# Kernel tuning notes

Measured on AMD Instinct MI355X. Metric: run time of the kernel, lower is better.

## Reference

```python
import jax, jax.numpy as jnp
import numpy as np


def setup_inputs() -> dict:
    key = jax.random.key(0)
    k1, k2, k3, k4, k5 = jax.random.split(key, 5)
    B, C, D = 16384, 1000, 2048
    x = jax.random.normal(k1, (B, D), dtype=jnp.float32)
    W = jax.random.normal(k2, (C, D), dtype=jnp.float32) * 0.02  # fc weight
    b = jax.random.normal(k3, (C,), dtype=jnp.float32) * 0.01
    selector_weights = jax.random.normal(k4, (5,), dtype=jnp.float32) * 0.01
    selector_thresholds = jax.random.normal(k5, (5,), dtype=jnp.float32) * 0.01
    ensemble_threshold = jnp.zeros((1,), dtype=jnp.float32)
    return {
        "x": x, "W": W, "b": b,
        "selector_weights": selector_weights,
        "selector_thresholds": selector_thresholds,
        "ensemble_threshold": ensemble_threshold,
    }


def _selector_scores(logits, W):
    # top-2 of raw logits (RLConfM): sorted descending -> top_k(2)
    top2, _ = jax.lax.top_k(logits, 2)
    conf_m = top2[:, 0] - top2[:, 1]
    # geometric margin (RLGeoM): logits normalized by row norms of fc weight
    w_norms = jnp.linalg.norm(W, axis=1)                      # [C]
    norm_logits = logits / (w_norms + 1e-8)[None, :]          # [B, C]
    ntop2, _ = jax.lax.top_k(norm_logits, 2)
    geo_m = ntop2[:, 0] - ntop2[:, 1]
    # softmax-based selectors share one softmax pass
    probs = jax.nn.softmax(logits, axis=1)                    # [B, C]
    sr_max = jnp.max(probs, axis=1)
    doctor = 1.0 - 1.0 / jnp.sum(probs * probs, axis=1)
    neg_entropy = jnp.sum(probs * jnp.log(probs + 1e-10), axis=1)  # = -entropy
    # order matches nn.ModuleList: [SRMax, SRDoctor, SREntropy, RLGeoM, RLConfM]
    return jnp.stack([sr_max, doctor, neg_entropy, geo_m, conf_m], axis=1)  # [B, 5]


def reference(x, W, b, selector_weights, selector_thresholds, ensemble_threshold):
    # base model runs under no_grad in the original
    logits = jax.lax.stop_gradient(jnp.dot(x, W.T) + b)       # [B, C]
    scores = _selector_scores(logits, jax.lax.stop_gradient(W))  # [B, 5]
    indicators = jnp.tanh(scores - selector_thresholds[None, :])  # [B, 5]
    ensemble = jnp.sum(selector_weights[None, :] * indicators, axis=1)  # [B]
    selection_score = jnp.tanh(ensemble - ensemble_threshold[0])
    return (logits, selection_score)
```

## Files before the change

kernel.cpp:

```cpp
#include <hip/hip_runtime.h>
#include <stdint.h>

#define B_ROWS 16384
#define C_COLS 1000
#define D_DIM  2048

typedef __bf16 bf16x8 __attribute__((ext_vector_type(8)));
typedef float  f32x4  __attribute__((ext_vector_type(4)));
typedef unsigned short u16;

__device__ __forceinline__ u16 f2bf(float f) {
  union { float f; uint32_t u; } v; v.f = f;
  return (u16)((v.u + 0x7FFFu + ((v.u >> 16) & 1u)) >> 16);
}

__global__ __launch_bounds__(256)
void prep(const float* __restrict__ W, const float* __restrict__ x,
          u16* __restrict__ Wb, u16* __restrict__ xb, float* __restrict__ norms) {
  const int r = blockIdx.x;
  const int t = threadIdx.x;
  const bool isW = (r < C_COLS);
  const float* src = isW ? (W + (size_t)r * D_DIM)
                         : (x + (size_t)(r - C_COLS) * D_DIM);
  u16* dst = isW ? (Wb + (size_t)r * D_DIM)
                 : (xb + (size_t)(r - C_COLS) * D_DIM);
  const int c = t * 8;
  float4 v0 = *reinterpret_cast<const float4*>(src + c);
  float4 v1 = *reinterpret_cast<const float4*>(src + c + 4);
  uint32_t p0 = (uint32_t)f2bf(v0.x) | ((uint32_t)f2bf(v0.y) << 16);
  uint32_t p1 = (uint32_t)f2bf(v0.z) | ((uint32_t)f2bf(v0.w) << 16);
  uint32_t p2 = (uint32_t)f2bf(v1.x) | ((uint32_t)f2bf(v1.y) << 16);
  uint32_t p3 = (uint32_t)f2bf(v1.z) | ((uint32_t)f2bf(v1.w) << 16);
  const int row_id = isW ? r : (r - C_COLS);
  const int m2 = (row_id & 7) << 3;
  uint4 val; val.x = p0; val.y = p1; val.z = p2; val.w = p3;
  *reinterpret_cast<uint4*>(dst + (c ^ m2)) = val;
  if (isW) {
    float ss = v0.x*v0.x + v0.y*v0.y + v0.z*v0.z + v0.w*v0.w
             + v1.x*v1.x + v1.y*v1.y + v1.z*v1.z + v1.w*v1.w;
    #pragma unroll
    for (int m = 32; m; m >>= 1) ss += __shfl_xor(ss, m);
    __shared__ float wss[4];
    if ((t & 63) == 0) wss[t >> 6] = ss;
    __syncthreads();
    if (t == 0) norms[r] = sqrtf(wss[0] + wss[1] + wss[2] + wss[3]);
  }
}

#define ABASE(B,H) (((B)*2+(H))*8192)
#define BBASE(B,H) (32768 + ((B)*2+(H))*8192)

#define STAGE_A(BUF,H,KT) { _Pragma("unroll") for (int j_=0;j_<2;++j_){ \
    const char* s_ = (const char*)xb + \
      (((size_t)(m0+(H)*128+j_*64+w*8+(l>>3)))*D_DIM + (KT)*64 + (l&7)*8)*2; \
    u16* d_ = lds + ABASE(BUF,H) + (j_*64 + w*8)*64; \
    __builtin_amdgcn_global_load_lds( \
      (const __attribute__((address_space(1))) void*)s_, \
      (__attribute__((address_space(3))) void*)d_, 16, 0, 0); } }

#define STAGE_B(BUF,H,KT) { _Pragma("unroll") for (int j_=0;j_<2;++j_){ \
    int gr_ = n0+(H)*128+j_*64+w*8+(l>>3); if (gr_ >= C_COLS) gr_ = C_COLS-1; \
    const char* s_ = (const char*)Wb + \
      (((size_t)gr_)*D_DIM + (KT)*64 + (l&7)*8)*2; \
    u16* d_ = lds + BBASE(BUF,H) + (j_*64 + w*8)*64; \
    __builtin_amdgcn_global_load_lds( \
      (const __attribute__((address_space(1))) void*)s_, \
      (__attribute__((address_space(3))) void*)d_, 16, 0, 0); } }

#define READ_A(BUF,MH) { _Pragma("unroll") for (int ks_=0;ks_<2;++ks_) \
  _Pragma("unroll") for (int fr_=0;fr_<4;++fr_){ \
    int ra_ = wr*64 + fr_*16 + (l&15); \
    int ca_ = (ks_*32 + ((l>>4)<<3)) ^ ((ra_&7)<<3); \
    Acur[ks_][fr_] = *reinterpret_cast<const bf16x8*>( \
        &lds[ABASE(BUF,MH) + ra_*64 + ca_]); } }

#define READ_B(BUF,NH,DST) { _Pragma("unroll") for (int ks_=0;ks_<2;++ks_) \
  _Pragma("unroll") for (int fc_=0;fc_<2;++fc_){ \
    int rb_ = wcn*32 + fc_*16 + (l&15); \
    int cb_ = (ks_*32 + ((l>>4)<<3)) ^ ((rb_&7)<<3); \
    DST[ks_][fc_] = *reinterpret_cast<const bf16x8*>( \
        &lds[BBASE(BUF,NH) + rb_*64 + cb_]); } }

#define MMA(MH,NH,BSRC) { \
  __builtin_amdgcn_s_setprio(1); \
  _Pragma("unroll") for (int ks_=0;ks_<2;++ks_) \
    _Pragma("unroll") for (int fr_=0;fr_<4;++fr_) \
      _Pragma("unroll") for (int fc_=0;fc_<2;++fc_) \
        acc[MH][fr_][NH][fc_] = __builtin_amdgcn_mfma_f32_16x16x32_bf16( \
            Acur[ks_][fr_], BSRC[ks_][fc_], acc[MH][fr_][NH][fc_], 0, 0, 0); \
  __builtin_amdgcn_s_setprio(0); }

#define BAR  __builtin_amdgcn_s_barrier()
#define LG0  asm volatile("s_waitcnt lgkmcnt(0)" ::: "memory")
#define LG8  asm volatile("s_waitcnt lgkmcnt(8)" ::: "memory")
#define SCHB __builtin_amdgcn_sched_barrier(0)
#define VM4  asm volatile("s_waitcnt vmcnt(4)" ::: "memory")
#define VM0  asm volatile("s_waitcnt vmcnt(0)" ::: "memory")

__global__ __launch_bounds__(512, 2)
void gemm8(const u16* __restrict__ xb, const u16* __restrict__ Wb,
           const float* __restrict__ bias, float* __restrict__ out) {
  __shared__ u16 lds[65536];

  const int bid = blockIdx.x;
  const int swz = (bid & 7) * 32 + (bid >> 3);
  const int tm = swz >> 2, tn = swz & 3;
  const int m0 = tm * 256, n0 = tn * 256;

  const int t = threadIdx.x, w = t >> 6, l = t & 63;
  const int wr = w >> 2, wcn = w & 3;

  f32x4 acc[2][4][2][2];
  #pragma unroll
  for (int a = 0; a < 2; ++a)
    #pragma unroll
    for (int b2 = 0; b2 < 4; ++b2)
      #pragma unroll
      for (int c2 = 0; c2 < 2; ++c2)
        #pragma unroll
        for (int d2 = 0; d2 < 2; ++d2)
          acc[a][b2][c2][d2] = (f32x4){0.f, 0.f, 0.f, 0.f};

  bf16x8 Acur[2][4], B0c[2][2], B1c[2][2];

  STAGE_A(0,0,0); STAGE_B(0,0,0); STAGE_A(0,1,0); STAGE_B(0,1,0);
  STAGE_A(1,0,1); STAGE_B(1,0,1);
  VM4;
  BAR;

  for (int it = 0; it < 15; ++it) {
    const int t1k = 2*it + 1, t2k = 2*it + 2, t3k = 2*it + 3;
    READ_A(0,0); READ_B(0,0,B0c); STAGE_A(1,1,t1k); LG8;
    BAR; LG0; SCHB; MMA(0,0,B0c); BAR;
    READ_B(0,1,B1c); STAGE_B(1,1,t1k);
    BAR; LG0; SCHB; MMA(0,1,B1c); BAR;
    READ_A(0,1); STAGE_A(0,0,t2k);
    BAR; LG0; SCHB; MMA(1,1,B1c); BAR;
    STAGE_B(0,0,t2k);
    BAR; SCHB; MMA(1,0,B0c); VM4; BAR;
    READ_A(1,0); READ_B(1,0,B0c); STAGE_A(0,1,t2k); LG8;
    BAR; LG0; SCHB; MMA(0,0,B0c); BAR;
    READ_B(1,1,B1c); STAGE_B(0,1,t2k);
    BAR; LG0; SCHB; MMA(0,1,B1c); BAR;
    READ_A(1,1); STAGE_A(1,0,t3k);
    BAR; LG0; SCHB; MMA(1,1,B1c); BAR;
    STAGE_B(1,0,t3k);
    BAR; SCHB; MMA(1,0,B0c); VM4; BAR;
  }
  READ_A(0,0); READ_B(0,0,B0c); STAGE_A(1,1,31); LG8;
  BAR; LG0; SCHB; MMA(0,0,B0c); BAR;
  READ_B(0,1,B1c); STAGE_B(1,1,31);
  BAR; LG0; SCHB; MMA(0,1,B1c); BAR;
  READ_A(0,1);
  BAR; LG0; SCHB; MMA(1,1,B1c); BAR;
  BAR; SCHB; MMA(1,0,B0c); VM0; BAR;
  READ_A(1,0); READ_B(1,0,B0c); LG8;
  BAR; LG0; SCHB; MMA(0,0,B0c); BAR;
  READ_B(1,1,B1c);
  BAR; LG0; SCHB; MMA(0,1,B1c); BAR;
  READ_A(1,1);
  BAR; LG0; SCHB; MMA(1,1,B1c); BAR;
  SCHB; MMA(1,0,B0c);

  #pragma unroll
  for (int mh = 0; mh < 2; ++mh)
    #pragma unroll
    for (int nh = 0; nh < 2; ++nh)
      #pragma unroll
      for (int fc = 0; fc < 2; ++fc) {
        int col = n0 + nh*128 + wcn*32 + fc*16 + (l & 15);
        if (col < C_COLS) {
          float bv = bias[col];
          #pragma unroll
          for (int fr = 0; fr < 4; ++fr) {
            int row0 = m0 + mh*128 + wr*64 + fr*16 + ((l >> 4) << 2);
            #pragma unroll
            for (int j = 0; j < 4; ++j)
              out[(size_t)(row0 + j) * C_COLS + col] = acc[mh][fr][nh][fc][j] + bv;
          }
        }
      }
}

__global__ __launch_bounds__(256)
void prep_w_fb(const float* __restrict__ W, u16* __restrict__ Wb,
               float* __restrict__ norms) {
  const int r = blockIdx.x;
  const int t = threadIdx.x;
  const float* row = W + (size_t)r * D_DIM;
  const int c = t * 8;
  float4 v0 = *reinterpret_cast<const float4*>(row + c);
  float4 v1 = *reinterpret_cast<const float4*>(row + c + 4);
  float ss = v0.x*v0.x + v0.y*v0.y + v0.z*v0.z + v0.w*v0.w
           + v1.x*v1.x + v1.y*v1.y + v1.z*v1.z + v1.w*v1.w;
  uint32_t p0 = (uint32_t)f2bf(v0.x) | ((uint32_t)f2bf(v0.y) << 16);
  uint32_t p1 = (uint32_t)f2bf(v0.z) | ((uint32_t)f2bf(v0.w) << 16);
  uint32_t p2 = (uint32_t)f2bf(v1.x) | ((uint32_t)f2bf(v1.y) << 16);
  uint32_t p3 = (uint32_t)f2bf(v1.z) | ((uint32_t)f2bf(v1.w) << 16);
  const int mask = (r & 7) << 3;
  uint4 val; val.x = p0; val.y = p1; val.z = p2; val.w = p3;
  *reinterpret_cast<uint4*>(Wb + (size_t)r * D_DIM + (c ^ mask)) = val;
  #pragma unroll
  for (int m = 32; m; m >>= 1) ss += __shfl_xor(ss, m);
  __shared__ float wss[4];
  if ((t & 63) == 0) wss[t >> 6] = ss;
  __syncthreads();
  if (t == 0) norms[r] = sqrtf(wss[0] + wss[1] + wss[2] + wss[3]);
}

__global__ __launch_bounds__(256)
void gemm_fb(const float* __restrict__ x, const u16* __restrict__ Wb,
             const float* __restrict__ bias, float* __restrict__ out) {
  __shared__ u16 lds[(128 + 128) * 64];
  const int bid = blockIdx.x;
  const int cpx = gridDim.x >> 3;
  const int swz = (bid & 7) * cpx + (bid >> 3);
  const int tn = swz & 7, tm = swz >> 3;
  const int m0 = tm * 128, n0 = tn * 128;
  const int t = threadIdx.x, w = t >> 6, l = t & 63;
  const int wr = w >> 1, wc = w & 1;
  f32x4 acc[4][4];
  #pragma unroll
  for (int i = 0; i < 4; ++i)
    #pragma unroll
    for (int j = 0; j < 4; ++j) acc[i][j] = (f32x4){0.f,0.f,0.f,0.f};
  const int ar = w * 32 + (l >> 4);
  const int ac4 = (l & 15) * 4;
  const float* aptr = x + (size_t)(m0 + ar) * D_DIM + ac4;
  for (int k0 = 0; k0 < D_DIM; k0 += 64) {
    #pragma unroll
    for (int i = 0; i < 4; ++i) {
      int ci = w * 4 + i;
      int br = ci * 8 + (l >> 3);
      int wrow = n0 + br; if (wrow >= C_COLS) wrow = C_COLS - 1;
      const char* src = (const char*)Wb + (size_t)wrow * (D_DIM * 2)
                        + k0 * 2 + (l & 7) * 16;
      u16* dst = lds + 128*64 + ci * 512;
      __builtin_amdgcn_global_load_lds(
          (const __attribute__((address_space(1))) void*)src,
          (__attribute__((address_space(3))) void*)dst, 16, 0, 0);
    }
    #pragma unroll
    for (int i = 0; i < 8; ++i) {
      int r = ar + i * 4;
      float4 v = *reinterpret_cast<const float4*>(aptr + (size_t)(i*4)*D_DIM + k0);
      ushort4 h;
      h.x = f2bf(v.x); h.y = f2bf(v.y); h.z = f2bf(v.z); h.w = f2bf(v.w);
      *reinterpret_cast<ushort4*>(&lds[r * 64 + (ac4 ^ ((r & 7) << 3))]) = h;
    }
    __syncthreads();
    #pragma unroll
    for (int kk = 0; kk < 64; kk += 32) {
      const int kg = kk + ((l >> 4) << 3);
      bf16x8 af[4], bfr[4];
      #pragma unroll
      for (int mi = 0; mi < 4; ++mi) {
        int row = wr * 64 + mi * 16 + (l & 15);
        af[mi] = *reinterpret_cast<const bf16x8*>(&lds[row*64 + (kg ^ ((row&7)<<3))]);
      }
      #pragma unroll
      for (int ni = 0; ni < 4; ++ni) {
        int row = wc * 64 + ni * 16 + (l & 15);
        bfr[ni] = *reinterpret_cast<const bf16x8*>(&lds[128*64 + row*64 + (kg ^ ((row&7)<<3))]);
      }
      #pragma unroll
      for (int mi = 0; mi < 4; ++mi)
        #pragma unroll
        for (int ni = 0; ni < 4; ++ni)
          acc[mi][ni] = __builtin_amdgcn_mfma_f32_16x16x32_bf16(
              af[mi], bfr[ni], acc[mi][ni], 0, 0, 0);
    }
    __syncthreads();
  }
  #pragma unroll
  for (int ni = 0; ni < 4; ++ni) {
    int col = n0 + wc * 64 + ni * 16 + (l & 15);
    if (col < C_COLS) {
      float bv = bias[col];
      #pragma unroll
      for (int mi = 0; mi < 4; ++mi) {
        int row0 = m0 + wr * 64 + mi * 16 + ((l >> 4) << 2);
        #pragma unroll
        for (int j = 0; j < 4; ++j)
          out[(size_t)(row0 + j) * C_COLS + col] = acc[mi][ni][j] + bv;
      }
    }
  }
}

__global__ __launch_bounds__(256)
void selector(const float* __restrict__ logits, const float* __restrict__ norms,
              const float* __restrict__ selw, const float* __restrict__ selt,
              const float* __restrict__ ethr, float* __restrict__ out) {
  __shared__ float nrm[1024];
  const int t = threadIdx.x;
  #pragma unroll
  for (int i = 0; i < 4; ++i) {
    int idx = t + i * 256;
    nrm[idx] = (idx < C_COLS) ? norms[idx] : 1.0f;
  }
  __syncthreads();

  const int w = t >> 6, l = t & 63;
  const int row = blockIdx.x * 4 + w;
  const float* lp = logits + (size_t)row * C_COLS;

  float lg[16];
  float t1 = -3.4e38f, t2 = -3.4e38f, n1 = -3.4e38f, n2 = -3.4e38f;
  #pragma unroll
  for (int i = 0; i < 4; ++i) {
    float4 v4 = *reinterpret_cast<const float4*>(lp + l * 4 + i * 256);
    #pragma unroll
    for (int j = 0; j < 4; ++j) {
      int idx = l * 4 + i * 256 + j;
      float raw = (j == 0) ? v4.x : (j == 1) ? v4.y : (j == 2) ? v4.z : v4.w;
      bool ok = (idx < C_COLS);
      float v = ok ? raw : -3.4e38f;
      lg[i * 4 + j] = v;
      if (v > t1) { t2 = t1; t1 = v; } else if (v > t2) t2 = v;
      float nv = ok ? raw / (nrm[idx] + 1e-8f) : -3.4e38f;
      if (nv > n1) { n2 = n1; n1 = nv; } else if (nv > n2) n2 = nv;
    }
  }
  #pragma unroll
  for (int m = 1; m < 64; m <<= 1) {
    float o1 = __shfl_xor(t1, m), o2 = __shfl_xor(t2, m);
    if (o1 > t1) { t2 = fmaxf(t1, o2); t1 = o1; } else t2 = fmaxf(t2, o1);
    float p1 = __shfl_xor(n1, m), p2 = __shfl_xor(n2, m);
    if (p1 > n1) { n2 = fmaxf(n1, p2); n1 = p1; } else n2 = fmaxf(n2, p1);
  }
  const float mx = t1;

  float S = 0.f, sq = 0.f;
  float ex[16];
  #pragma unroll
  for (int i = 0; i < 16; ++i) {
    float e = (lg[i] > -1e38f) ? __expf(lg[i] - mx) : 0.f;
    ex[i] = e; S += e; sq += e * e;
  }
  #pragma unroll
  for (int m = 1; m < 64; m <<= 1) { S += __shfl_xor(S, m); sq += __shfl_xor(sq, m); }

  float ent = 0.f;
  #pragma unroll
  for (int i = 0; i < 16; ++i) {
    if (lg[i] > -1e38f) {
      float p = ex[i] / S;
      ent += p * __logf(p + 1e-10f);
    }
  }
  #pragma unroll
  for (int m = 1; m < 64; m <<= 1) ent += __shfl_xor(ent, m);

  if (l == 0) {
    float sc0 = 1.f / S;
    float sc1 = 1.f - (S * S) / sq;
    float sc2 = ent;
    float sc3 = n1 - n2;
    float sc4 = t1 - t2;
    float ens = selw[0] * tanhf(sc0 - selt[0])
              + selw[1] * tanhf(sc1 - selt[1])
              + selw[2] * tanhf(sc2 - selt[2])
              + selw[3] * tanhf(sc3 - selt[3])
              + selw[4] * tanhf(sc4 - selt[4]);
    out[row] = tanhf(ens - ethr[0]);
  }
}

extern "C" void kernel_launch(void* const* d_in, const int* in_sizes, int n_in,
                              void* d_out, int out_size, void* d_ws, size_t ws_size,
                              hipStream_t stream) {
  const float* x    = (const float*)d_in[0];
  const float* W    = (const float*)d_in[1];
  const float* b    = (const float*)d_in[2];
  const float* selw = (const float*)d_in[3];
  const float* selt = (const float*)d_in[4];
  const float* ethr = (const float*)d_in[5];
  float* out = (float*)d_out;

  u16*   Wb    = (u16*)d_ws;
  float* norms = (float*)((char*)d_ws + 4096000);
  u16*   xb    = (u16*)((char*)d_ws + 4100096);
  const size_t need = 4100096 + (size_t)B_ROWS * D_DIM * 2;

  if (ws_size >= need) {
    prep<<<C_COLS + B_ROWS, 256, 0, stream>>>(W, x, Wb, xb, norms);
    gemm8<<<256, 512, 0, stream>>>(xb, Wb, b, out);
  } else {
    prep_w_fb<<<C_COLS, 256, 0, stream>>>(W, Wb, norms);
    gemm_fb<<<(B_ROWS / 128) * 8, 256, 0, stream>>>(x, Wb, b, out);
  }
  selector<<<B_ROWS / 4, 256, 0, stream>>>(out, norms, selw, selt, ethr,
                                           out + (size_t)B_ROWS * C_COLS);
}
```

Measured before the change: 133.4 us.

## Fuse fp32-to-bf16 conversion of x into GEMM register-staged A loads

```diff
diff --git a/kernel.cpp b/kernel.cpp
--- a/kernel.cpp
+++ b/kernel.cpp
@@ -15,48 +15,49 @@
 }
 
 __global__ __launch_bounds__(256)
-void prep(const float* __restrict__ W, const float* __restrict__ x,
-          u16* __restrict__ Wb, u16* __restrict__ xb, float* __restrict__ norms) {
+void prep_w(const float* __restrict__ W, u16* __restrict__ Wb,
+            float* __restrict__ norms) {
   const int r = blockIdx.x;
   const int t = threadIdx.x;
-  const bool isW = (r < C_COLS);
-  const float* src = isW ? (W + (size_t)r * D_DIM)
-                         : (x + (size_t)(r - C_COLS) * D_DIM);
-  u16* dst = isW ? (Wb + (size_t)r * D_DIM)
-                 : (xb + (size_t)(r - C_COLS) * D_DIM);
+  const float* row = W + (size_t)r * D_DIM;
   const int c = t * 8;
-  float4 v0 = *reinterpret_cast<const float4*>(src + c);
-  float4 v1 = *reinterpret_cast<const float4*>(src + c + 4);
+  float4 v0 = *reinterpret_cast<const float4*>(row + c);
+  float4 v1 = *reinterpret_cast<const float4*>(row + c + 4);
+  float ss = v0.x*v0.x + v0.y*v0.y + v0.z*v0.z + v0.w*v0.w
+           + v1.x*v1.x + v1.y*v1.y + v1.z*v1.z + v1.w*v1.w;
   uint32_t p0 = (uint32_t)f2bf(v0.x) | ((uint32_t)f2bf(v0.y) << 16);
   uint32_t p1 = (uint32_t)f2bf(v0.z) | ((uint32_t)f2bf(v0.w) << 16);
   uint32_t p2 = (uint32_t)f2bf(v1.x) | ((uint32_t)f2bf(v1.y) << 16);
   uint32_t p3 = (uint32_t)f2bf(v1.z) | ((uint32_t)f2bf(v1.w) << 16);
-  const int row_id = isW ? r : (r - C_COLS);
-  const int m2 = (row_id & 7) << 3;
+  const int mask = (r & 7) << 3;
   uint4 val; val.x = p0; val.y = p1; val.z = p2; val.w = p3;
-  *reinterpret_cast<uint4*>(dst + (c ^ m2)) = val;
-  if (isW) {
-    float ss = v0.x*v0.x + v0.y*v0.y + v0.z*v0.z + v0.w*v0.w
-             + v1.x*v1.x + v1.y*v1.y + v1.z*v1.z + v1.w*v1.w;
-    #pragma unroll
-    for (int m = 32; m; m >>= 1) ss += __shfl_xor(ss, m);
-    __shared__ float wss[4];
-    if ((t & 63) == 0) wss[t >> 6] = ss;
-    __syncthreads();
-    if (t == 0) norms[r] = sqrtf(wss[0] + wss[1] + wss[2] + wss[3]);
-  }
+  *reinterpret_cast<uint4*>(Wb + (size_t)r * D_DIM + (c ^ mask)) = val;
+  #pragma unroll
+  for (int m = 32; m; m >>= 1) ss += __shfl_xor(ss, m);
+  __shared__ float wss[4];
+  if ((t & 63) == 0) wss[t >> 6] = ss;
+  __syncthreads();
+  if (t == 0) norms[r] = sqrtf(wss[0] + wss[1] + wss[2] + wss[3]);
 }
 
 #define ABASE(B,H) (((B)*2+(H))*8192)
 #define BBASE(B,H) (32768 + ((B)*2+(H))*8192)
 
-#define STAGE_A(BUF,H,KT) { _Pragma("unroll") for (int j_=0;j_<2;++j_){ \
-    const char* s_ = (const char*)xb + \
-      (((size_t)(m0+(H)*128+j_*64+w*8+(l>>3)))*D_DIM + (KT)*64 + (l&7)*8)*2; \
-    u16* d_ = lds + ABASE(BUF,H) + (j_*64 + w*8)*64; \
-    __builtin_amdgcn_global_load_lds( \
-      (const __attribute__((address_space(1))) void*)s_, \
-      (__attribute__((address_space(3))) void*)d_, 16, 0, 0); } }
+#define ISSUE_A(SET,H,KT) { _Pragma("unroll") for (int j_=0;j_<2;++j_){ \
+    const float* s_ = x + (size_t)(m0+(H)*128+j_*64+w*8+(l>>3))*D_DIM \
+                        + (KT)*64 + (l&7)*8; \
+    SET[2*j_]   = *reinterpret_cast<const float4*>(s_); \
+    SET[2*j_+1] = *reinterpret_cast<const float4*>(s_ + 4); } }
+
+#define WRITE_A(SET,BUF,H) { _Pragma("unroll") for (int j_=0;j_<2;++j_){ \
+    int r_ = j_*64 + w*8 + (l>>3); \
+    bf16x8 h_; \
+    h_[0]=(__bf16)SET[2*j_].x;   h_[1]=(__bf16)SET[2*j_].y; \
+    h_[2]=(__bf16)SET[2*j_].z;   h_[3]=(__bf16)SET[2*j_].w; \
+    h_[4]=(__bf16)SET[2*j_+1].x; h_[5]=(__bf16)SET[2*j_+1].y; \
+    h_[6]=(__bf16)SET[2*j_+1].z; h_[7]=(__bf16)SET[2*j_+1].w; \
+    *reinterpret_cast<bf16x8*>(&lds[ABASE(BUF,H) + r_*64 + \
+        (((l&7)*8) ^ ((r_&7)<<3))]) = h_; } }
 
 #define STAGE_B(BUF,H,KT) { _Pragma("unroll") for (int j_=0;j_<2;++j_){ \
     int gr_ = n0+(H)*128+j_*64+w*8+(l>>3); if (gr_ >= C_COLS) gr_ = C_COLS-1; \
@@ -98,7 +99,7 @@
 #define VM0  asm volatile("s_waitcnt vmcnt(0)" ::: "memory")
 
 __global__ __launch_bounds__(512, 2)
-void gemm8(const u16* __restrict__ xb, const u16* __restrict__ Wb,
+void gemm8(const float* __restrict__ x, const u16* __restrict__ Wb,
            const float* __restrict__ bias, float* __restrict__ out) {
   __shared__ u16 lds[65536];
 
@@ -122,32 +123,37 @@
           acc[a][b2][c2][d2] = (f32x4){0.f, 0.f, 0.f, 0.f};
 
   bf16x8 Acur[2][4], B0c[2][2], B1c[2][2];
-
-  STAGE_A(0,0,0); STAGE_B(0,0,0); STAGE_A(0,1,0); STAGE_B(0,1,0);
-  STAGE_A(1,0,1); STAGE_B(1,0,1);
+  float4 aIss0[4], aIss1[4];
+
+  ISSUE_A(aIss0, 0, 0); WRITE_A(aIss0, 0, 0);
+  ISSUE_A(aIss0, 1, 0); WRITE_A(aIss0, 0, 1);
+  ISSUE_A(aIss0, 0, 1); WRITE_A(aIss0, 1, 0);
+  STAGE_B(0,0,0); STAGE_B(0,1,0); STAGE_B(1,0,1);
+  ISSUE_A(aIss1, 1, 1);
   VM4;
+  LG0;
   BAR;
 
   for (int it = 0; it < 15; ++it) {
-    const int t1k = 2*it + 1, t2k = 2*it + 2, t3k = 2*it + 3;
-    READ_A(0,0); READ_B(0,0,B0c); STAGE_A(1,1,t1k); LG8;
+    const int t2k = 2*it + 2, t3k = 2*it + 3;
+    READ_A(0,0); READ_B(0,0,B0c); WRITE_A(aIss1,1,1); ISSUE_A(aIss0,0,t2k); LG8;
     BAR; LG0; SCHB; MMA(0,0,B0c); BAR;
-    READ_B(0,1,B1c); STAGE_B(1,1,t1k);
+    READ_B(0,1,B1c); STAGE_B(1,1,2*it+1);
     BAR; LG0; SCHB; MMA(0,1,B1c); BAR;
-    READ_A(0,1); STAGE_A(0,0,t2k);
+    READ_A(0,1); WRITE_A(aIss0,0,0); ISSUE_A(aIss1,1,t2k);
     BAR; LG0; SCHB; MMA(1,1,B1c); BAR;
     STAGE_B(0,0,t2k);
     BAR; SCHB; MMA(1,0,B0c); VM4; BAR;
-    READ_A(1,0); READ_B(1,0,B0c); STAGE_A(0,1,t2k); LG8;
+    READ_A(1,0); READ_B(1,0,B0c); WRITE_A(aIss1,0,1); ISSUE_A(aIss0,0,t3k); LG8;
     BAR; LG0; SCHB; MMA(0,0,B0c); BAR;
     READ_B(1,1,B1c); STAGE_B(0,1,t2k);
     BAR; LG0; SCHB; MMA(0,1,B1c); BAR;
-    READ_A(1,1); STAGE_A(1,0,t3k);
+    READ_A(1,1); WRITE_A(aIss0,1,0); ISSUE_A(aIss1,1,t3k);
     BAR; LG0; SCHB; MMA(1,1,B1c); BAR;
     STAGE_B(1,0,t3k);
     BAR; SCHB; MMA(1,0,B0c); VM4; BAR;
   }
-  READ_A(0,0); READ_B(0,0,B0c); STAGE_A(1,1,31); LG8;
+  READ_A(0,0); READ_B(0,0,B0c); WRITE_A(aIss1,1,1); LG8;
   BAR; LG0; SCHB; MMA(0,0,B0c); BAR;
   READ_B(0,1,B1c); STAGE_B(1,1,31);
   BAR; LG0; SCHB; MMA(0,1,B1c); BAR;
@@ -183,112 +189,6 @@
 }
 
 __global__ __launch_bounds__(256)
-void prep_w_fb(const float* __restrict__ W, u16* __restrict__ Wb,
-               float* __restrict__ norms) {
-  const int r = blockIdx.x;
-  const int t = threadIdx.x;
-  const float* row = W + (size_t)r * D_DIM;
-  const int c = t * 8;
-  float4 v0 = *reinterpret_cast<const float4*>(row + c);
-  float4 v1 = *reinterpret_cast<const float4*>(row + c + 4);
-  float ss = v0.x*v0.x + v0.y*v0.y + v0.z*v0.z + v0.w*v0.w
-           + v1.x*v1.x + v1.y*v1.y + v1.z*v1.z + v1.w*v1.w;
-  uint32_t p0 = (uint32_t)f2bf(v0.x) | ((uint32_t)f2bf(v0.y) << 16);
-  uint32_t p1 = (uint32_t)f2bf(v0.z) | ((uint32_t)f2bf(v0.w) << 16);
-  uint32_t p2 = (uint32_t)f2bf(v1.x) | ((uint32_t)f2bf(v1.y) << 16);
-  uint32_t p3 = (uint32_t)f2bf(v1.z) | ((uint32_t)f2bf(v1.w) << 16);
-  const int mask = (r & 7) << 3;
-  uint4 val; val.x = p0; val.y = p1; val.z = p2; val.w = p3;
-  *reinterpret_cast<uint4*>(Wb + (size_t)r * D_DIM + (c ^ mask)) = val;
-  #pragma unroll
-  for (int m = 32; m; m >>= 1) ss += __shfl_xor(ss, m);
-  __shared__ float wss[4];
-  if ((t & 63) == 0) wss[t >> 6] = ss;
-  __syncthreads();
-  if (t == 0) norms[r] = sqrtf(wss[0] + wss[1] + wss[2] + wss[3]);
-}
-
-__global__ __launch_bounds__(256)
-void gemm_fb(const float* __restrict__ x, const u16* __restrict__ Wb,
-             const float* __restrict__ bias, float* __restrict__ out) {
-  __shared__ u16 lds[(128 + 128) * 64];
-  const int bid = blockIdx.x;
-  const int cpx = gridDim.x >> 3;
-  const int swz = (bid & 7) * cpx + (bid >> 3);
-  const int tn = swz & 7, tm = swz >> 3;
-  const int m0 = tm * 128, n0 = tn * 128;
-  const int t = threadIdx.x, w = t >> 6, l = t & 63;
-  const int wr = w >> 1, wc = w & 1;
-  f32x4 acc[4][4];
-  #pragma unroll
-  for (int i = 0; i < 4; ++i)
-    #pragma unroll
-    for (int j = 0; j < 4; ++j) acc[i][j] = (f32x4){0.f,0.f,0.f,0.f};
-  const int ar = w * 32 + (l >> 4);
-  const int ac4 = (l & 15) * 4;
-  const float* aptr = x + (size_t)(m0 + ar) * D_DIM + ac4;
-  for (int k0 = 0; k0 < D_DIM; k0 += 64) {
-    #pragma unroll
-    for (int i = 0; i < 4; ++i) {
-      int ci = w * 4 + i;
-      int br = ci * 8 + (l >> 3);
-      int wrow = n0 + br; if (wrow >= C_COLS) wrow = C_COLS - 1;
-      const char* src = (const char*)Wb + (size_t)wrow * (D_DIM * 2)
-                        + k0 * 2 + (l & 7) * 16;
-      u16* dst = lds + 128*64 + ci * 512;
-      __builtin_amdgcn_global_load_lds(
-          (const __attribute__((address_space(1))) void*)src,
-          (__attribute__((address_space(3))) void*)dst, 16, 0, 0);
-    }
-    #pragma unroll
-    for (int i = 0; i < 8; ++i) {
-      int r = ar + i * 4;
-      float4 v = *reinterpret_cast<const float4*>(aptr + (size_t)(i*4)*D_DIM + k0);
-      ushort4 h;
-      h.x = f2bf(v.x); h.y = f2bf(v.y); h.z = f2bf(v.z); h.w = f2bf(v.w);
-      *reinterpret_cast<ushort4*>(&lds[r * 64 + (ac4 ^ ((r & 7) << 3))]) = h;
-    }
-    __syncthreads();
-    #pragma unroll
-    for (int kk = 0; kk < 64; kk += 32) {
-      const int kg = kk + ((l >> 4) << 3);
-      bf16x8 af[4], bfr[4];
-      #pragma unroll
-      for (int mi = 0; mi < 4; ++mi) {
-        int row = wr * 64 + mi * 16 + (l & 15);
-        af[mi] = *reinterpret_cast<const bf16x8*>(&lds[row*64 + (kg ^ ((row&7)<<3))]);
-      }
-      #pragma unroll
-      for (int ni = 0; ni < 4; ++ni) {
-        int row = wc * 64 + ni * 16 + (l & 15);
-        bfr[ni] = *reinterpret_cast<const bf16x8*>(&lds[128*64 + row*64 + (kg ^ ((row&7)<<3))]);
-      }
-      #pragma unroll
-      for (int mi = 0; mi < 4; ++mi)
-        #pragma unroll
-        for (int ni = 0; ni < 4; ++ni)
-          acc[mi][ni] = __builtin_amdgcn_mfma_f32_16x16x32_bf16(
-              af[mi], bfr[ni], acc[mi][ni], 0, 0, 0);
-    }
-    __syncthreads();
-  }
-  #pragma unroll
-  for (int ni = 0; ni < 4; ++ni) {
-    int col = n0 + wc * 64 + ni * 16 + (l & 15);
-    if (col < C_COLS) {
-      float bv = bias[col];
-      #pragma unroll
-      for (int mi = 0; mi < 4; ++mi) {
-        int row0 = m0 + wr * 64 + mi * 16 + ((l >> 4) << 2);
-        #pragma unroll
-        for (int j = 0; j < 4; ++j)
-          out[(size_t)(row0 + j) * C_COLS + col] = acc[mi][ni][j] + bv;
-      }
-    }
-  }
-}
-
-__global__ __launch_bounds__(256)
 void selector(const float* __restrict__ logits, const float* __restrict__ norms,
               const float* __restrict__ selw, const float* __restrict__ selt,
               const float* __restrict__ ethr, float* __restrict__ out) {
@@ -380,16 +280,9 @@
 
   u16*   Wb    = (u16*)d_ws;
   float* norms = (float*)((char*)d_ws + 4096000);
-  u16*   xb    = (u16*)((char*)d_ws + 4100096);
-  const size_t need = 4100096 + (size_t)B_ROWS * D_DIM * 2;
-
-  if (ws_size >= need) {
-    prep<<<C_COLS + B_ROWS, 256, 0, stream>>>(W, x, Wb, xb, norms);
-    gemm8<<<256, 512, 0, stream>>>(xb, Wb, b, out);
-  } else {
-    prep_w_fb<<<C_COLS, 256, 0, stream>>>(W, Wb, norms);
-    gemm_fb<<<(B_ROWS / 128) * 8, 256, 0, stream>>>(x, Wb, b, out);
-  }
+
+  prep_w<<<C_COLS, 256, 0, stream>>>(W, Wb, norms);
+  gemm8<<<256, 512, 0, stream>>>(x, Wb, b, out);
   selector<<<B_ROWS / 4, 256, 0, stream>>>(out, norms, selw, selt, ethr,
                                            out + (size_t)B_ROWS * C_COLS);
 }
```

After: 155.9 us. 16.9% more time.

## Fuse selector partial reductions into GEMM epilogue with online softmax merge

Applied to the files above, without the earlier changes.

```diff
diff --git a/kernel.cpp b/kernel.cpp
--- a/kernel.cpp
+++ b/kernel.cpp
@@ -97,9 +97,22 @@
 #define VM4  asm volatile("s_waitcnt vmcnt(4)" ::: "memory")
 #define VM0  asm volatile("s_waitcnt vmcnt(0)" ::: "memory")
 
+#define SMERGE(m_,s_,q_,u_,om_,os_,oq_,ou_) { \
+    float M_ = fmaxf(m_, om_); \
+    float a_ = __expf(m_ - M_), b_ = __expf(om_ - M_); \
+    float ns_ = a_*s_ + b_*os_; \
+    float nq_ = a_*a_*q_ + b_*b_*oq_; \
+    float nu_ = a_*(u_ + (m_-M_)*s_) + b_*(ou_ + (om_-M_)*os_); \
+    m_ = M_; s_ = ns_; q_ = nq_; u_ = nu_; }
+
+#define T2MERGE(t1_,t2_,o1_,o2_) { \
+    if (o1_ > t1_) { t2_ = fmaxf(t1_, o2_); t1_ = o1_; } else t2_ = fmaxf(t2_, o1_); }
+
+template<int FUSE>
 __global__ __launch_bounds__(512, 2)
 void gemm8(const u16* __restrict__ xb, const u16* __restrict__ Wb,
-           const float* __restrict__ bias, float* __restrict__ out) {
+           const float* __restrict__ bias, float* __restrict__ out,
+           const float* __restrict__ norms, float* __restrict__ partials) {
   __shared__ u16 lds[65536];
 
   const int bid = blockIdx.x;
@@ -162,130 +175,144 @@
   BAR; LG0; SCHB; MMA(1,1,B1c); BAR;
   SCHB; MMA(1,0,B0c);
 
+  float bv[2][2], nvn[2][2]; bool okc[2][2];
+  #pragma unroll
+  for (int nh = 0; nh < 2; ++nh)
+    #pragma unroll
+    for (int fc = 0; fc < 2; ++fc) {
+      int col = n0 + nh*128 + wcn*32 + fc*16 + (l & 15);
+      okc[nh][fc] = (col < C_COLS);
+      bv[nh][fc]  = okc[nh][fc] ? bias[col] : 0.f;
+      nvn[nh][fc] = okc[nh][fc] ? (norms[col] + 1e-8f) : 1.f;
+    }
+
   #pragma unroll
   for (int mh = 0; mh < 2; ++mh)
     #pragma unroll
     for (int nh = 0; nh < 2; ++nh)
       #pragma unroll
-      for (int fc = 0; fc < 2; ++fc) {
-        int col = n0 + nh*128 + wcn*32 + fc*16 + (l & 15);
-        if (col < C_COLS) {
-          float bv = bias[col];
+      for (int fc = 0; fc < 2; ++fc)
+        if (okc[nh][fc]) {
+          int col = n0 + nh*128 + wcn*32 + fc*16 + (l & 15);
           #pragma unroll
           for (int fr = 0; fr < 4; ++fr) {
             int row0 = m0 + mh*128 + wr*64 + fr*16 + ((l >> 4) << 2);
             #pragma unroll
             for (int j = 0; j < 4; ++j)
-              out[(size_t)(row0 + j) * C_COLS + col] = acc[mh][fr][nh][fc][j] + bv;
+              out[(size_t)(row0 + j) * C_COLS + col] = acc[mh][fr][nh][fc][j] + bv[nh][fc];
           }
         }
+
+  if constexpr (FUSE) {
+    float* sf = (float*)lds;
+    BAR;
+    #pragma unroll
+    for (int mh = 0; mh < 2; ++mh)
+      #pragma unroll
+      for (int fr = 0; fr < 4; ++fr)
+        #pragma unroll
+        for (int j = 0; j < 4; ++j) {
+          float t1=-3.4e38f, t2=-3.4e38f, n1=-3.4e38f, n2=-3.4e38f, m=-3.4e38f;
+          float vv[2][2];
+          #pragma unroll
+          for (int nh = 0; nh < 2; ++nh)
+            #pragma unroll
+            for (int fc = 0; fc < 2; ++fc) {
+              float v = acc[mh][fr][nh][fc][j] + bv[nh][fc];
+              vv[nh][fc] = v;
+              if (okc[nh][fc]) {
+                if (v > t1) { t2 = t1; t1 = v; } else if (v > t2) t2 = v;
+                float nv = v / nvn[nh][fc];
+                if (nv > n1) { n2 = n1; n1 = nv; } else if (nv > n2) n2 = nv;
+                m = fmaxf(m, v);
+              }
+            }
+          float s = 0.f, q = 0.f, u = 0.f;
+          #pragma unroll
+          for (int nh = 0; nh < 2; ++nh)
+            #pragma unroll
+            for (int fc = 0; fc < 2; ++fc)
+              if (okc[nh][fc]) {
+                float d = vv[nh][fc] - m;
+                float e = __expf(d);
+                s += e; q += e*e; u += d*e;
+              }
+          #pragma unroll
+          for (int msk = 1; msk < 16; msk <<= 1) {
+            float o1 = __shfl_xor(t1, msk), o2 = __shfl_xor(t2, msk);
+            T2MERGE(t1, t2, o1, o2);
+            float p1 = __shfl_xor(n1, msk), p2 = __shfl_xor(n2, msk);
+            T2MERGE(n1, n2, p1, p2);
+            float om = __shfl_xor(m, msk), os = __shfl_xor(s, msk);
+            float oq = __shfl_xor(q, msk), ou = __shfl_xor(u, msk);
+            SMERGE(m, s, q, u, om, os, oq, ou);
+          }
+          int row_local = mh*128 + wr*64 + fr*16 + ((l >> 4) << 2) + j;
+          int k = l & 15;
+          if (k < 8) {
+            float pv = (k==0)?t1:(k==1)?t2:(k==2)?n1:(k==3)?n2:
+                       (k==4)?m :(k==5)?s :(k==6)?q : u;
+            sf[(wcn*256 + row_local)*9 + k] = pv;
+          }
+        }
+    BAR;
+    if (t < 256) {
+      float P[4][8];
+      #pragma unroll
+      for (int wv = 0; wv < 4; ++wv)
+        #pragma unroll
+        for (int k = 0; k < 8; ++k)
+          P[wv][k] = sf[(wv*256 + t)*9 + k];
+      float t1=P[0][0], t2=P[0][1], n1=P[0][2], n2=P[0][3];
+      float m=P[0][4], s=P[0][5], q=P[0][6], u=P[0][7];
+      #pragma unroll
+      for (int wv = 1; wv < 4; ++wv) {
+        T2MERGE(t1, t2, P[wv][0], P[wv][1]);
+        T2MERGE(n1, n2, P[wv][2], P[wv][3]);
+        SMERGE(m, s, q, u, P[wv][4], P[wv][5], P[wv][6], P[wv][7]);
       }
+      float* pp = partials + ((size_t)(m0 + t) * 4 + tn) * 8;
+      float4 lo; lo.x=t1; lo.y=t2; lo.z=n1; lo.w=n2;
+      float4 hi; hi.x=m;  hi.y=s;  hi.z=q;  hi.w=u;
+      *reinterpret_cast<float4*>(pp)     = lo;
+      *reinterpret_cast<float4*>(pp + 4) = hi;
+    }
+  }
 }
 
 __global__ __launch_bounds__(256)
-void prep_w_fb(const float* __restrict__ W, u16* __restrict__ Wb,
-               float* __restrict__ norms) {
-  const int r = blockIdx.x;
-  const int t = threadIdx.x;
-  const float* row = W + (size_t)r * D_DIM;
-  const int c = t * 8;
-  float4 v0 = *reinterpret_cast<const float4*>(row + c);
-  float4 v1 = *reinterpret_cast<const float4*>(row + c + 4);
-  float ss = v0.x*v0.x + v0.y*v0.y + v0.z*v0.z + v0.w*v0.w
-           + v1.x*v1.x + v1.y*v1.y + v1.z*v1.z + v1.w*v1.w;
-  uint32_t p0 = (uint32_t)f2bf(v0.x) | ((uint32_t)f2bf(v0.y) << 16);
-  uint32_t p1 = (uint32_t)f2bf(v0.z) | ((uint32_t)f2bf(v0.w) << 16);
-  uint32_t p2 = (uint32_t)f2bf(v1.x) | ((uint32_t)f2bf(v1.y) << 16);
-  uint32_t p3 = (uint32_t)f2bf(v1.z) | ((uint32_t)f2bf(v1.w) << 16);
-  const int mask = (r & 7) << 3;
-  uint4 val; val.x = p0; val.y = p1; val.z = p2; val.w = p3;
-  *reinterpret_cast<uint4*>(Wb + (size_t)r * D_DIM + (c ^ mask)) = val;
-  #pragma unroll
-  for (int m = 32; m; m >>= 1) ss += __shfl_xor(ss, m);
-  __shared__ float wss[4];
-  if ((t & 63) == 0) wss[t >> 6] = ss;
-  __syncthreads();
-  if (t == 0) norms[r] = sqrtf(wss[0] + wss[1] + wss[2] + wss[3]);
-}
-
-__global__ __launch_bounds__(256)
-void gemm_fb(const float* __restrict__ x, const u16* __restrict__ Wb,
-             const float* __restrict__ bias, float* __restrict__ out) {
-  __shared__ u16 lds[(128 + 128) * 64];
-  const int bid = blockIdx.x;
-  const int cpx = gridDim.x >> 3;
-  const int swz = (bid & 7) * cpx + (bid >> 3);
-  const int tn = swz & 7, tm = swz >> 3;
-  const int m0 = tm * 128, n0 = tn * 128;
-  const int t = threadIdx.x, w = t >> 6, l = t & 63;
-  const int wr = w >> 1, wc = w & 1;
-  f32x4 acc[4][4];
-  #pragma unroll
-  for (int i = 0; i < 4; ++i)
-    #pragma unroll
-    for (int j = 0; j < 4; ++j) acc[i][j] = (f32x4){0.f,0.f,0.f,0.f};
-  const int ar = w * 32 + (l >> 4);
-  const int ac4 = (l & 15) * 4;
-  const float* aptr = x + (size_t)(m0 + ar) * D_DIM + ac4;
-  for (int k0 = 0; k0 < D_DIM; k0 += 64) {
-    #pragma unroll
-    for (int i = 0; i < 4; ++i) {
-      int ci = w * 4 + i;
-      int br = ci * 8 + (l >> 3);
-      int wrow = n0 + br; if (wrow >= C_COLS) wrow = C_COLS - 1;
-      const char* src = (const char*)Wb + (size_t)wrow * (D_DIM * 2)
-                        + k0 * 2 + (l & 7) * 16;
-      u16* dst = lds + 128*64 + ci * 512;
-      __builtin_amdgcn_global_load_lds(
-          (const __attribute__((address_space(1))) void*)src,
-          (__attribute__((address_space(3))) void*)dst, 16, 0, 0);
-    }
-    #pragma unroll
-    for (int i = 0; i < 8; ++i) {
-      int r = ar + i * 4;
-      float4 v = *reinterpret_cast<const float4*>(aptr + (size_t)(i*4)*D_DIM + k0);
-      ushort4 h;
-      h.x = f2bf(v.x); h.y = f2bf(v.y); h.z = f2bf(v.z); h.w = f2bf(v.w);
-      *reinterpret_cast<ushort4*>(&lds[r * 64 + (ac4 ^ ((r & 7) << 3))]) = h;
-    }
-    __syncthreads();
-    #pragma unroll
-    for (int kk = 0; kk < 64; kk += 32) {
-      const int kg = kk + ((l >> 4) << 3);
-      bf16x8 af[4], bfr[4];
-      #pragma unroll
-      for (int mi = 0; mi < 4; ++mi) {
-        int row = wr * 64 + mi * 16 + (l & 15);
-        af[mi] = *reinterpret_cast<const bf16x8*>(&lds[row*64 + (kg ^ ((row&7)<<3))]);
-      }
-      #pragma unroll
-      for (int ni = 0; ni < 4; ++ni) {
-        int row = wc * 64 + ni * 16 + (l & 15);
-        bfr[ni] = *reinterpret_cast<const bf16x8*>(&lds[128*64 + row*64 + (kg ^ ((row&7)<<3))]);
-      }
-      #pragma unroll
-      for (int mi = 0; mi < 4; ++mi)
-        #pragma unroll
-        for (int ni = 0; ni < 4; ++ni)
-          acc[mi][ni] = __builtin_amdgcn_mfma_f32_16x16x32_bf16(
-              af[mi], bfr[ni], acc[mi][ni], 0, 0, 0);
-    }
-    __syncthreads();
-  }
-  #pragma unroll
-  for (int ni = 0; ni < 4; ++ni) {
-    int col = n0 + wc * 64 + ni * 16 + (l & 15);
-    if (col < C_COLS) {
-      float bv = bias[col];
-      #pragma unroll
-      for (int mi = 0; mi < 4; ++mi) {
-        int row0 = m0 + wr * 64 + mi * 16 + ((l >> 4) << 2);
-        #pragma unroll
-        for (int j = 0; j < 4; ++j)
-          out[(size_t)(row0 + j) * C_COLS + col] = acc[mi][ni][j] + bv;
-      }
-    }
-  }
+void selector2(const float* __restrict__ partials,
+               const float* __restrict__ selw, const float* __restrict__ selt,
+               const float* __restrict__ ethr, float* __restrict__ out2) {
+  const int row = blockIdx.x * 256 + threadIdx.x;
+  const float* pp = partials + (size_t)row * 32;
+  float P[4][8];
+  #pragma unroll
+  for (int wv = 0; wv < 4; ++wv) {
+    float4 lo = *reinterpret_cast<const float4*>(pp + wv*8);
+    float4 hi = *reinterpret_cast<const float4*>(pp + wv*8 + 4);
+    P[wv][0]=lo.x; P[wv][1]=lo.y; P[wv][2]=lo.z; P[wv][3]=lo.w;
+    P[wv][4]=hi.x; P[wv][5]=hi.y; P[wv][6]=hi.z; P[wv][7]=hi.w;
+  }
+  float t1=P[0][0], t2=P[0][1], n1=P[0][2], n2=P[0][3];
+  float m=P[0][4], s=P[0][5], q=P[0][6], u=P[0][7];
+  #pragma unroll
+  for (int wv = 1; wv < 4; ++wv) {
+    T2MERGE(t1, t2, P[wv][0], P[wv][1]);
+    T2MERGE(n1, n2, P[wv][2], P[wv][3]);
+    SMERGE(m, s, q, u, P[wv][4], P[wv][5], P[wv][6], P[wv][7]);
+  }
+  float sc0 = 1.f / s;
+  float sc1 = 1.f - (s * s) / q;
+  float sc2 = u / s - __logf(s);
+  float sc3 = n1 - n2;
+  float sc4 = t1 - t2;
+  float ens = selw[0] * tanhf(sc0 - selt[0])
+            + selw[1] * tanhf(sc1 - selt[1])
+            + selw[2] * tanhf(sc2 - selt[2])
+            + selw[3] * tanhf(sc3 - selt[3])
+            + selw[4] * tanhf(sc4 - selt[4]);
+  out2[row] = tanhf(ens - ethr[0]);
 }
 
 __global__ __launch_bounds__(256)
@@ -300,11 +327,9 @@
     nrm[idx] = (idx < C_COLS) ? norms[idx] : 1.0f;
   }
   __syncthreads();
-
   const int w = t >> 6, l = t & 63;
   const int row = blockIdx.x * 4 + w;
   const float* lp = logits + (size_t)row * C_COLS;
-
   float lg[16];
   float t1 = -3.4e38f, t2 = -3.4e38f, n1 = -3.4e38f, n2 = -3.4e38f;
   #pragma unroll
@@ -325,12 +350,11 @@
   #pragma unroll
   for (int m = 1; m < 64; m <<= 1) {
     float o1 = __shfl_xor(t1, m), o2 = __shfl_xor(t2, m);
-    if (o1 > t1) { t2 = fmaxf(t1, o2); t1 = o1; } else t2 = fmaxf(t2, o1);
+    T2MERGE(t1, t2, o1, o2);
     float p1 = __shfl_xor(n1, m), p2 = __shfl_xor(n2, m);
-    if (p1 > n1) { n2 = fmaxf(n1, p2); n1 = p1; } else n2 = fmaxf(n2, p1);
+    T2MERGE(n1, n2, p1, p2);
   }
   const float mx = t1;
-
   float S = 0.f, sq = 0.f;
   float ex[16];
   #pragma unroll
@@ -340,29 +364,18 @@
   }
   #pragma unroll
   for (int m = 1; m < 64; m <<= 1) { S += __shfl_xor(S, m); sq += __shfl_xor(sq, m); }
-
   float ent = 0.f;
   #pragma unroll
-  for (int i = 0; i < 16; ++i) {
-    if (lg[i] > -1e38f) {
-      float p = ex[i] / S;
-      ent += p * __logf(p + 1e-10f);
-    }
-  }
+  for (int i = 0; i < 16; ++i)
+    if (lg[i] > -1e38f) { float p = ex[i] / S; ent += p * __logf(p + 1e-10f); }
   #pragma unroll
   for (int m = 1; m < 64; m <<= 1) ent += __shfl_xor(ent, m);
-
   if (l == 0) {
-    float sc0 = 1.f / S;
-    float sc1 = 1.f - (S * S) / sq;
-    float sc2 = ent;
-    float sc3 = n1 - n2;
-    float sc4 = t1 - t2;
-    float ens = selw[0] * tanhf(sc0 - selt[0])
-              + selw[1] * tanhf(sc1 - selt[1])
-              + selw[2] * tanhf(sc2 - selt[2])
-              + selw[3] * tanhf(sc3 - selt[3])
-              + selw[4] * tanhf(sc4 - selt[4]);
+    float ens = selw[0] * tanhf(1.f / S - selt[0])
+              + selw[1] * tanhf(1.f - (S * S) / sq - selt[1])
+              + selw[2] * tanhf(ent - selt[2])
+              + selw[3] * tanhf(n1 - n2 - selt[3])
+              + selw[4] * tanhf(t1 - t2 - selt[4]);
     out[row] = tanhf(ens - ethr[0]);
   }
 }
@@ -377,19 +390,23 @@
   const float* selt = (const float*)d_in[4];
   const float* ethr = (const float*)d_in[5];
   float* out = (float*)d_out;
+  float* out2 = out + (size_t)B_ROWS * C_COLS;
 
   u16*   Wb    = (u16*)d_ws;
   float* norms = (float*)((char*)d_ws + 4096000);
   u16*   xb    = (u16*)((char*)d_ws + 4100096);
-  const size_t need = 4100096 + (size_t)B_ROWS * D_DIM * 2;
-
-  if (ws_size >= need) {
+  float* parts = (float*)((char*)d_ws + 4100096 + 67108864);
+
+  const size_t need_fuse = 4100096 + 67108864 + 2097152;
+  const size_t need_r4   = 4100096 + 67108864;
+
+  if (ws_size >= need_fuse) {
     prep<<<C_COLS + B_ROWS, 256, 0, stream>>>(W, x, Wb, xb, norms);
-    gemm8<<<256, 512, 0, stream>>>(xb, Wb, b, out);
-  } else {
-    prep_w_fb<<<C_COLS, 256, 0, stream>>>(W, Wb, norms);
-    gemm_fb<<<(B_ROWS / 128) * 8, 256, 0, stream>>>(x, Wb, b, out);
-  }
-  selector<<<B_ROWS / 4, 256, 0, stream>>>(out, norms, selw, selt, ethr,
-                                           out + (size_t)B_ROWS * C_COLS);
-}
+    gemm8<1><<<256, 512, 0, stream>>>(xb, Wb, b, out, norms, parts);
+    selector2<<<B_ROWS / 256, 256, 0, stream>>>(parts, selw, selt, ethr, out2);
+  } else if (ws_size >= need_r4) {
+    prep<<<C_COLS + B_ROWS, 256, 0, stream>>>(W, x, Wb, xb, norms);
+    gemm8<0><<<256, 512, 0, stream>>>(xb, Wb, b, out, norms, nullptr);
+    selector<<<B_ROWS / 4, 256, 0, stream>>>(out, norms, selw, selt, ethr, out2);
+  }
+}
```

Result: slower. 148.5 us (+11.3%).
